# Kernel tuning notes

Measured on AMD Instinct MI355X. Metric: run time of the kernel, lower is better.

Reference implementation:

```python
import jax, jax.numpy as jnp
import numpy as np


def setup_inputs() -> dict:
    key = jax.random.key(0)
    ks = jax.random.split(key, 8)
    B, S, P = 512, 128, 32            # batch, seq_len, pred_len
    F, O, H = 64, 64, 1024            # feat_dim, label/output_dim, hidden_dim
    IN = F + O                        # GRUCell input_dim = 128
    w = 0.05                          # weight scale to keep gates in useful range
    return {
        "feats": jax.random.normal(ks[0], (B, S + P - 1, F), jnp.float32),
        "labels": jax.random.normal(ks[1], (B, S, O), jnp.float32),
        "Wi": jax.random.normal(ks[2], (3 * H, IN), jnp.float32) * w,
        "Wh": jax.random.normal(ks[3], (3 * H, H), jnp.float32) * w,
        "bi": jax.random.normal(ks[4], (3 * H,), jnp.float32) * w,
        "bh": jax.random.normal(ks[5], (3 * H,), jnp.float32) * w,
        "Wd": jax.random.normal(ks[6], (O, H), jnp.float32) * w,
        "bd": jax.random.normal(ks[7], (O,), jnp.float32) * w,
    }


def _gru_cell(h, x, Wi, Wh, bi, bh):
    # torch.nn.GRUCell semantics
    gi = x @ Wi.T + bi                       # [B, 3H]
    gh = h @ Wh.T + bh                       # [B, 3H]
    i_r, i_z, i_n = jnp.split(gi, 3, axis=-1)
    h_r, h_z, h_n = jnp.split(gh, 3, axis=-1)
    r = jax.nn.sigmoid(i_r + h_r)
    z = jax.nn.sigmoid(i_z + h_z)
    n = jnp.tanh(i_n + r * h_n)
    return (1.0 - z) * n + z * h


def reference(feats, labels, Wi, Wh, bi, bh, Wd, bd):
    B, S, O = labels.shape
    H = Wh.shape[1]
    prior = feats[:, :S]                     # [B, S, F]
    post = feats[:, S:]                      # [B, P-1, F]
    x = jnp.concatenate([prior, labels], axis=-1)   # [B, S, F+O]

    h0 = jnp.zeros((B, H), feats.dtype)

    def enc_step(h, xt):
        return _gru_cell(h, xt, Wi, Wh, bi, bh), None

    h, _ = jax.lax.scan(enc_step, h0, jnp.swapaxes(x, 0, 1))

    ps = h @ Wd.T + bd                       # decoder output [B, O]

    def dec_step(carry, ft):
        h, ps = carry
        xin = jnp.concatenate([ft, ps], axis=-1)
        h = _gru_cell(h, xin, Wi, Wh, bi, bh)
        ps = h @ Wd.T + bd
        return (h, ps), ps

    _, rest = jax.lax.scan(dec_step, (h, ps), jnp.swapaxes(post, 0, 1))
    return jnp.concatenate([ps[None], rest], axis=0)  # [pred_len, B, O]
```

## Files before the change

kernel.cpp:

```cpp
#include <hip/hip_runtime.h>
#include <cstdint>
#include <cstddef>

#define SENC  128
#define NSTEPS 159
#define HB16  524288
#define XSLICE 131072
#define SLAB_ELEMS 55296
#define FRAG_TOTAL 442368
#define FS 16

typedef short  short8  __attribute__((ext_vector_type(8)));
typedef float  floatx4 __attribute__((ext_vector_type(4)));
typedef float  f32x4   __attribute__((ext_vector_type(4)));
typedef int    i32x4   __attribute__((ext_vector_type(4)));
typedef unsigned long long u64;

#define MFMA(a, b, c) __builtin_amdgcn_mfma_f32_16x16x32_bf16((a), (b), (c), 0, 0, 0)

__device__ __forceinline__ i32x4 ld_nc16(const void* p) {
    i32x4 r;
    asm volatile("global_load_dwordx4 %0, %1, off sc0 sc1" : "=&v"(r) : "v"(p) : "memory");
    return r;
}
__device__ __forceinline__ i32x4 ld_sc0_16(const void* p) {
    i32x4 r;
    asm volatile("global_load_dwordx4 %0, %1, off sc0" : "=&v"(r) : "v"(p) : "memory");
    return r;
}
__device__ __forceinline__ void st_swap8(void* p, u64 v) {
    asm volatile("global_atomic_swap_x2 %0, %1, off sc1" :: "v"(p), "v"(v) : "memory");
}
__device__ __forceinline__ void st_swap4(void* p, unsigned v) {
    asm volatile("global_atomic_swap %0, %1, off sc1" :: "v"(p), "v"(v) : "memory");
}
#define WAITVM(N) asm volatile("s_waitcnt vmcnt(" #N ")" ::: "memory")
#define WAITLGKM  asm volatile("s_waitcnt lgkmcnt(0)" ::: "memory")

__device__ __forceinline__ unsigned ldu_dev(const unsigned* p) {
    return __hip_atomic_load(p, __ATOMIC_RELAXED, __HIP_MEMORY_SCOPE_AGENT);
}
__device__ __forceinline__ u64 ldq_dev(const u64* p) {
    return __hip_atomic_load(p, __ATOMIC_RELAXED, __HIP_MEMORY_SCOPE_AGENT);
}
__device__ __forceinline__ void stu_dev(unsigned* p, unsigned v) {
    __hip_atomic_store(p, v, __ATOMIC_RELAXED, __HIP_MEMORY_SCOPE_AGENT);
}

__device__ __forceinline__ unsigned ld_ws(const unsigned* p) {
    return __hip_atomic_load(p, __ATOMIC_RELAXED, __HIP_MEMORY_SCOPE_WORKGROUP);
}
__device__ __forceinline__ void st_ws(unsigned* p, unsigned v) {
    __hip_atomic_store(p, v, __ATOMIC_RELAXED, __HIP_MEMORY_SCOPE_WORKGROUP);
}
__device__ __forceinline__ unsigned add_ws(unsigned* p, unsigned v) {
    return __hip_atomic_fetch_add(p, v, __ATOMIC_RELAXED, __HIP_MEMORY_SCOPE_WORKGROUP);
}

__device__ __forceinline__ float bf2f(short s) {
    return __uint_as_float(((unsigned)(unsigned short)s) << 16);
}
__device__ __forceinline__ short f2bf(float f) {
    unsigned u = __float_as_uint(f);
    return (short)((u + 0x7FFFu + ((u >> 16) & 1u)) >> 16);
}
__device__ __forceinline__ void f2pair(float f, short& hi, short& lo) {
    hi = f2bf(f);
    lo = f2bf(f - bf2f(hi));
}

__device__ __forceinline__ float sigm(float x) {
    return 1.0f / (1.0f + __expf(-x));
}
__device__ __forceinline__ float tanh_fast(float x) {
    float cx = fminf(fmaxf(x, -15.0f), 15.0f);
    float e = __expf(2.0f * cx);
    return (e - 1.0f) / (e + 1.0f);
}

__global__ void setup_swizzle(const float* __restrict__ Wi, const float* __restrict__ Wh,
                              short* __restrict__ whi, short* __restrict__ wlo_x) {
    const int idx = blockIdx.x * 256 + threadIdx.x;
    if (idx >= FRAG_TOTAL) return;
    const int l    = idx & 63;
    const int rest = idx >> 6;
    const int t    = rest % 3;
    const int ki   = (rest / 3) % 36;
    const int c    = rest / 108;
    const int nrow = t * 1024 + c * 16 + (l & 15);
    const int kb   = ki * 32 + (l >> 4) * 8;
    short8 vh, vl;
#pragma unroll
    for (int j = 0; j < 8; ++j) {
        const int k = kb + j;
        float w = (k < 128) ? Wi[(size_t)nrow * 128 + k]
                            : Wh[(size_t)nrow * 1024 + (k - 128)];
        short h, lo2;
        f2pair(w, h, lo2);
        vh[j] = h; vl[j] = lo2;
    }
    *(short8*)(whi + (size_t)idx * 8) = vh;
    if (ki < 4) {
        const int xi = ((c * 4 + ki) * 3 + t) * 64 + l;
        *(short8*)(wlo_x + (size_t)xi * 8) = vl;
    }
}

#define HCONS(S, KI) do { \
    short8 ah_ = *(short8*)&hb[S]; \
    const int fo_ = (((KI) * 3) * 64 + lane) * 8; \
    short8 b0_ = *(const short8*)(s_whi + fo_); \
    short8 b1_ = *(const short8*)(s_whi + fo_ + 512); \
    short8 b2_ = *(const short8*)(s_whi + fo_ + 1024); \
    aR  = MFMA(ah_, b0_, aR); \
    aZ  = MFMA(ah_, b1_, aZ); \
    aNh = MFMA(ah_, b2_, aNh); \
} while (0)

#define CH_ISSUE(LDFN, B, KC) do { \
    const short* hp_ = hrd + (size_t)(KC) * 16384; \
    hb[(B) + 0] = LDFN(hp_); \
    hb[(B) + 1] = LDFN(hp_ + 4096); \
    hb[(B) + 2] = LDFN(hp_ + 8192); \
    hb[(B) + 3] = LDFN(hp_ + 12288); \
} while (0)

#define CH_CONS(B, KC) do { \
    const int kb_ = 4 + 4 * (KC); \
    HCONS((B) + 0, kb_ + 0); \
    HCONS((B) + 1, kb_ + 1); \
    HCONS((B) + 2, kb_ + 2); \
    HCONS((B) + 3, kb_ + 3); \
} while (0)

#define SPIN_CH(KC) do { \
    while (ld_ws(&s_sub[KC]) < (unsigned)step) __builtin_amdgcn_s_sleep(2); \
} while (0)

#define REGION2(LDFN) do { \
    i32x4 hb[16]; \
    const int k0_ = r0;            const int k1_ = (r0 + 1) & 7; \
    const int k2_ = (r0 + 2) & 7;  const int k3_ = (r0 + 3) & 7; \
    const int k4_ = (r0 + 4) & 7;  const int k5_ = (r0 + 5) & 7; \
    const int k6_ = (r0 + 6) & 7;  const int k7_ = (r0 + 7) & 7; \
    SPIN_CH(k0_); CH_ISSUE(LDFN, 0,  k0_); \
    SPIN_CH(k1_); CH_ISSUE(LDFN, 4,  k1_); \
    SPIN_CH(k2_); CH_ISSUE(LDFN, 8,  k2_); \
    SPIN_CH(k3_); CH_ISSUE(LDFN, 12, k3_); \
    WAITVM(12); CH_CONS(0,  k0_); SPIN_CH(k4_); CH_ISSUE(LDFN, 0,  k4_); \
    WAITVM(12); CH_CONS(4,  k1_); SPIN_CH(k5_); CH_ISSUE(LDFN, 4,  k5_); \
    WAITVM(12); CH_CONS(8,  k2_); SPIN_CH(k6_); CH_ISSUE(LDFN, 8,  k6_); \
    WAITVM(12); CH_CONS(12, k3_); SPIN_CH(k7_); CH_ISSUE(LDFN, 12, k7_); \
    WAITVM(12); CH_CONS(0,  k4_); \
    WAITVM(8);  CH_CONS(4,  k5_); \
    WAITVM(4);  CH_CONS(8,  k6_); \
    WAITVM(0);  CH_CONS(12, k7_); \
} while (0)

#define R1TRIPLE(KI) do { \
    short8 ah_, al_; \
    _Pragma("unroll") \
    for (int j = 0; j < 8; ++j) { short h2_, l2_; f2pair(f[j], h2_, l2_); ah_[j] = h2_; al_[j] = l2_; } \
    const int fo_ = (((KI) * 3) * 64 + lane) * 8; \
    short8 b0_ = *(const short8*)(s_whi + fo_); \
    short8 b1_ = *(const short8*)(s_whi + fo_ + 512); \
    short8 b2_ = *(const short8*)(s_whi + fo_ + 1024); \
    aR  = MFMA(ah_, b0_, aR);  aR  = MFMA(ah_, L0r[KI], aR);  aR  = MFMA(al_, b0_, aR); \
    aZ  = MFMA(ah_, b1_, aZ);  aZ  = MFMA(ah_, L1r[KI], aZ);  aZ  = MFMA(al_, b1_, aZ); \
    aNi = MFMA(ah_, b2_, aNi); aNi = MFMA(ah_, L2r[KI], aNi); aNi = MFMA(al_, b2_, aNi); \
} while (0)

#define LOADF(KI) do { \
    const float* s_ = feats + ((size_t)brow * 159 + step) * 64 + (KI) * 32 + q * 8; \
    f32x4 a_ = ((const f32x4*)s_)[0], b_ = ((const f32x4*)s_)[1]; \
    _Pragma("unroll") for (int j = 0; j < 4; ++j) { f[j] = a_[j]; f[4 + j] = b_[j]; } \
} while (0)

#define LOADL(KI) do { \
    const float* s_ = labels + ((size_t)brow * 128 + step) * 64 + ((KI) - 2) * 32 + q * 8; \
    f32x4 a_ = ((const f32x4*)s_)[0], b_ = ((const f32x4*)s_)[1]; \
    _Pragma("unroll") for (int j = 0; j < 4; ++j) { f[j] = a_[j]; f[4 + j] = b_[j]; } \
} while (0)

#define LOADP(KI) do { \
    const u64* pp_ = (const u64*)(ps_f32 + (size_t)brow * 64 + ((KI) - 2) * 32 + q * 8); \
    _Pragma("unroll") for (int j = 0; j < 4; ++j) { \
        u64 v_ = ldq_dev(pp_ + j); \
        f[2 * j]     = __uint_as_float((unsigned)v_); \
        f[2 * j + 1] = __uint_as_float((unsigned)(v_ >> 32)); } \
} while (0)

__global__ __launch_bounds__(512, 2) void gru_main(
    const float* __restrict__ feats, const float* __restrict__ labels,
    const float* __restrict__ bi,    const float* __restrict__ bh,
    const float* __restrict__ Wd,    const float* __restrict__ bd,
    const short* __restrict__ whi_sw, const short* __restrict__ wlo_x,
    short* __restrict__ h16,         float* __restrict__ ps_f32,
    float* __restrict__ out,
    unsigned* __restrict__ hflag,
    unsigned* __restrict__ pflag,
    int nslots)
{
    __shared__ short s_whi[SLAB_ELEMS];
    __shared__ float s_ps[2048];
    __shared__ short s_tr[8][16][18];
    __shared__ unsigned s_sub[8];
    __shared__ unsigned s_arrD, s_arrI;

    const int tid  = threadIdx.x;
    const int lane = tid & 63;
    const int wv   = tid >> 6;
    const int q    = lane >> 4;
    const int n16  = lane & 15;
    const int c    = blockIdx.x & 63;
    const int r    = blockIdx.x >> 6;
    const int r0   = c & 7;
    const bool cached = (nslots > 2);

    if (tid < 8) s_sub[tid] = 0;
    if (tid == 8) s_arrD = 0;
    if (tid == 9) s_arrI = 0;
    {
        const f32x4* src = (const f32x4*)(whi_sw + (size_t)c * SLAB_ELEMS);
        f32x4* dst = (f32x4*)s_whi;
        for (int i = tid; i < SLAB_ELEMS / 8; i += 512) dst[i] = src[i];
    }
    __syncthreads();

    const int mbase = r * 128 + wv * 16;
    const int brow  = mbase + n16;
    const int row_r = c * 16 + n16;
    const float bias_r  = bi[row_r] + bh[row_r];
    const float bias_z  = bi[1024 + row_r] + bh[1024 + row_r];
    const float bias_ni = bi[2048 + row_r];
    const float bias_nh = bh[2048 + row_r];

    unsigned* my_hflag = hflag + (r * 64 + c) * FS;
    unsigned* my_pflag = pflag + (r * 64 + c) * FS;
    const unsigned* hfp     = hflag + (r * 64 + 8 * wv + (lane & 7)) * FS;
    const unsigned* pfp     = pflag + (r * 64 + 8 * wv + (lane & 7)) * FS;
    const unsigned* grp_hfl = hflag + (r * 64) * FS;

    short8 L0r[4], L1r[4], L2r[4];
#pragma unroll
    for (int ki = 0; ki < 4; ++ki) {
        const short* base = wlo_x + (size_t)(((c * 4 + ki) * 3) * 64 + lane) * 8;
        L0r[ki] = *(const short8*)(base);
        L1r[ki] = *(const short8*)(base + 512);
        L2r[ki] = *(const short8*)(base + 1024);
    }

    float hold[4] = {0.f, 0.f, 0.f, 0.f};

    for (int step = 0; step < NSTEPS; ++step) {
        const bool dec = (step >= SENC);
        const unsigned tgt = (unsigned)(step + 1);
        const int rslot = cached ? step       : (step & 1);
        const int wslot = cached ? (step + 1) : ((step + 1) & 1);
        const short* hrd = h16 + (size_t)rslot * HB16 + (size_t)r * XSLICE
                         + (size_t)(wv * 16 + n16) * 16 + (q & 1) * 8 + (q >> 1) * 2048;
        short* hwr = h16 + (size_t)wslot * HB16 + (size_t)r * XSLICE;

        unsigned pf_pre = 0xFFFFFFFFu;
        if (dec) pf_pre = ldu_dev(pfp);

        floatx4 aR  = (floatx4){bias_r,  bias_r,  bias_r,  bias_r};
        floatx4 aZ  = (floatx4){bias_z,  bias_z,  bias_z,  bias_z};
        floatx4 aNi = (floatx4){bias_ni, bias_ni, bias_ni, bias_ni};
        floatx4 aNh = (floatx4){bias_nh, bias_nh, bias_nh, bias_nh};

        {
            float f[8];
            LOADF(0); R1TRIPLE(0);
            LOADF(1); R1TRIPLE(1);

            if (step > 0 && step <= SENC - 1) {
                WAITVM(0);
                if (lane == 0) {
                    unsigned old = add_ws(&s_arrD, 1u);
                    if (old == 8u * (unsigned)step - 1u)
                        stu_dev(my_hflag, (unsigned)step);
                }
            }

            if (!dec) {
                LOADL(2); R1TRIPLE(2);
                LOADL(3); R1TRIPLE(3);
            } else {
                if (!__all(pf_pre >= (unsigned)step)) {
                    while (!__all(ldu_dev(pfp) >= (unsigned)step))
                        __builtin_amdgcn_s_sleep(2);
                }
                LOADP(2); R1TRIPLE(2);
                LOADP(3); R1TRIPLE(3);
            }
        }

        if (step > 0) {
            if (!dec) {
                while (!__all(ldu_dev(hfp) >= (unsigned)step))
                    __builtin_amdgcn_s_sleep(2);
            }
            if (lane == 0) st_ws(&s_sub[wv], (unsigned)step);
            if (cached) { REGION2(ld_sc0_16); }
            else        { REGION2(ld_nc16); }
        }

        {
#pragma unroll
            for (int i = 0; i < 4; ++i) {
                float rr = sigm(aR[i]);
                float zz = sigm(aZ[i]);
                float nn = tanh_fast(aNi[i] + rr * aNh[i]);
                float hv = (1.0f - zz) * nn + zz * hold[i];
                hold[i] = hv;
                s_tr[wv][q * 4 + i][n16] = f2bf(hv);
            }
            WAITLGKM;
            const int rr2 = lane >> 2, seg = lane & 3;
            u64 v = *(const u64*)&s_tr[wv][rr2][seg * 4];
            st_swap8(hwr + (size_t)c * 2048 + (size_t)(wv * 16 + rr2) * 16 + seg * 4, v);
            if (step >= SENC - 1) {
                WAITVM(0);
                if (lane == 0) {
                    unsigned old = add_ws(&s_arrI, 1u);
                    if (old == 8u * (unsigned)(step - (SENC - 1) + 1) - 1u)
                        stu_dev(my_hflag, tgt);
                }
            }
        }

        if (step >= SENC - 1) {
            const int ot = step - (SENC - 1);
            const int prow0 = r * 128 + 2 * c;
            if (wv == 0) {
                while (ldu_dev(grp_hfl + lane * FS) < tgt)
                    __builtin_amdgcn_s_sleep(2);
            }
            __syncthreads();
            if (tid < 256) {
                const int rl = tid >> 7, rest = tid & 127;
                const int ct = rest >> 1, half = rest & 1;
                const short* src = hwr + (size_t)ct * 2048
                                 + (size_t)(2 * c + rl) * 16 + half * 8;
                i32x4 v = ld_nc16(src);
                WAITVM(0);
                short8 s = *(short8*)&v;
#pragma unroll
                for (int j = 0; j < 8; ++j)
                    s_ps[rl * 1024 + ct * 16 + half * 8 + j] = bf2f(s[j]);
            }
            __syncthreads();
            const int o = tid >> 3, e = tid & 7;
            const float* wrow = Wd + (size_t)o * 1024;
            float acc0 = 0.0f, acc1 = 0.0f;
#pragma unroll 8
            for (int j = 0; j < 32; ++j) {
                const int k = j * 32 + e * 4;
                f32x4 w  = *(const f32x4*)(wrow + k);
                f32x4 a4 = *(const f32x4*)(s_ps + k);
                f32x4 b4 = *(const f32x4*)(s_ps + 1024 + k);
                acc0 += a4[0] * w[0] + a4[1] * w[1] + a4[2] * w[2] + a4[3] * w[3];
                acc1 += b4[0] * w[0] + b4[1] * w[1] + b4[2] * w[2] + b4[3] * w[3];
            }
            acc0 += __shfl_xor(acc0, 1); acc0 += __shfl_xor(acc0, 2); acc0 += __shfl_xor(acc0, 4);
            acc1 += __shfl_xor(acc1, 1); acc1 += __shfl_xor(acc1, 2); acc1 += __shfl_xor(acc1, 4);
            if (e == 0) {
                float v0 = acc0 + bd[o];
                float v1 = acc1 + bd[o];
                out[((size_t)ot * 512 + prow0)     * 64 + o] = v0;
                out[((size_t)ot * 512 + prow0 + 1) * 64 + o] = v1;
                st_swap4(ps_f32 + (size_t)prow0       * 64 + o, __float_as_uint(v0));
                st_swap4(ps_f32 + (size_t)(prow0 + 1) * 64 + o, __float_as_uint(v1));
            }
            WAITVM(0);
            __syncthreads();
            if (tid == 0) stu_dev(my_pflag, tgt);
        }
    }
}

extern "C" void kernel_launch(void* const* d_in, const int* in_sizes, int n_in,
                              void* d_out, int out_size, void* d_ws, size_t ws_size,
                              hipStream_t stream) {
    const float* feats  = (const float*)d_in[0];
    const float* labels = (const float*)d_in[1];
    const float* Wi     = (const float*)d_in[2];
    const float* Wh     = (const float*)d_in[3];
    const float* bi     = (const float*)d_in[4];
    const float* bh     = (const float*)d_in[5];
    const float* Wd     = (const float*)d_in[6];
    const float* bd     = (const float*)d_in[7];
    float* out = (float*)d_out;

    char* ws = (char*)d_ws;
    short*    whi_sw = (short*)(ws);
    short*    wlo_x  = (short*)(ws + 7077888);
    float*    ps_f32 = (float*)(ws + 7864320);
    unsigned* pflag  = (unsigned*)(ws + 7995392);
    unsigned* hflag  = (unsigned*)(ws + 8011776);
    short*    h16    = (short*)(ws + 8388608);

    const size_t need = 8388608ull + 160ull * 1048576ull;
    int nslots = (ws_size >= need) ? 160 : 2;

    hipMemsetAsync(ws + 7995392, 0, 32768, stream);

    setup_swizzle<<<FRAG_TOTAL / 256, 256, 0, stream>>>(Wi, Wh, whi_sw, wlo_x);

    void* args[] = {(void*)&feats, (void*)&labels, (void*)&bi, (void*)&bh,
                    (void*)&Wd, (void*)&bd, (void*)&whi_sw, (void*)&wlo_x,
                    (void*)&h16, (void*)&ps_f32, (void*)&out,
                    (void*)&hflag, (void*)&pflag, (void*)&nslots};
    hipLaunchCooperativeKernel(reinterpret_cast<void*>(gru_main),
                               dim3(256), dim3(512), args, 0, stream);
}
```

Before: 1.410 ms.

## Split each block into two independent wave chains with per-chain flags

```diff
diff --git a/kernel.cpp b/kernel.cpp
--- a/kernel.cpp
+++ b/kernel.cpp
@@ -134,7 +134,7 @@
 } while (0)
 
 #define SPIN_CH(KC) do { \
-    while (ld_ws(&s_sub[KC]) < (unsigned)step) __builtin_amdgcn_s_sleep(2); \
+    while (ld_ws(&s_sub2[CHN][(KC) >> 1]) < (unsigned)step) __builtin_amdgcn_s_sleep(2); \
 } while (0)
 
 #define REGION2(LDFN) do { \
@@ -190,6 +190,12 @@
         f[2 * j + 1] = __uint_as_float((unsigned)(v_ >> 32)); } \
 } while (0)
 
+#define CHAIN_SYNC() do { \
+    cs_tgt += 4u; \
+    if (lane == 0) add_ws(&s_cs[CHN], 1u); \
+    while (ld_ws(&s_cs[CHN]) < cs_tgt) __builtin_amdgcn_s_sleep(1); \
+} while (0)
+
 __global__ __launch_bounds__(512, 2) void gru_main(
     const float* __restrict__ feats, const float* __restrict__ labels,
     const float* __restrict__ bi,    const float* __restrict__ bh,
@@ -204,28 +210,39 @@
     __shared__ short s_whi[SLAB_ELEMS];
     __shared__ float s_ps[2048];
     __shared__ short s_tr[8][16][18];
-    __shared__ unsigned s_sub[8];
-    __shared__ unsigned s_arrD, s_arrI;
+    __shared__ unsigned s_sub2[2][4];
+    __shared__ unsigned s_arrD2[2];
+    __shared__ unsigned s_arrI2[2];
+    __shared__ unsigned s_cs[2];
 
     const int tid  = threadIdx.x;
     const int lane = tid & 63;
     const int wv   = tid >> 6;
+    const int CHN  = wv >> 2;
+    const int wv4  = wv & 3;
     const int q    = lane >> 4;
     const int n16  = lane & 15;
     const int c    = blockIdx.x & 63;
     const int r    = blockIdx.x >> 6;
     const int r0   = c & 7;
     const bool cached = (nslots > 2);
-
-    if (tid < 8) s_sub[tid] = 0;
-    if (tid == 8) s_arrD = 0;
-    if (tid == 9) s_arrI = 0;
+    unsigned cs_tgt = 0;
+
+    if (tid < 8)   s_sub2[tid >> 2][tid & 3] = 0;
+    if (tid == 8)  s_arrD2[0] = 0;
+    if (tid == 9)  s_arrD2[1] = 0;
+    if (tid == 10) s_arrI2[0] = 0;
+    if (tid == 11) s_arrI2[1] = 0;
+    if (tid == 12) s_cs[0] = 0;
+    if (tid == 13) s_cs[1] = 0;
     {
         const f32x4* src = (const f32x4*)(whi_sw + (size_t)c * SLAB_ELEMS);
         f32x4* dst = (f32x4*)s_whi;
         for (int i = tid; i < SLAB_ELEMS / 8; i += 512) dst[i] = src[i];
     }
     __syncthreads();
+
+    if (CHN == 1) { __builtin_amdgcn_s_sleep(127); __builtin_amdgcn_s_sleep(32); }
 
     const int mbase = r * 128 + wv * 16;
     const int brow  = mbase + n16;
@@ -235,11 +252,10 @@
     const float bias_ni = bi[2048 + row_r];
     const float bias_nh = bh[2048 + row_r];
 
-    unsigned* my_hflag = hflag + (r * 64 + c) * FS;
+    unsigned* my_hflag = hflag + (((r * 64 + c) * 2) + CHN) * FS;
     unsigned* my_pflag = pflag + (r * 64 + c) * FS;
-    const unsigned* hfp     = hflag + (r * 64 + 8 * wv + (lane & 7)) * FS;
-    const unsigned* pfp     = pflag + (r * 64 + 8 * wv + (lane & 7)) * FS;
-    const unsigned* grp_hfl = hflag + (r * 64) * FS;
+    const unsigned* hfp16 = hflag + (((r * 64 + 16 * wv4 + (lane & 15)) * 2) + CHN) * FS;
+    const unsigned* pfp   = pflag + (r * 64 + 8 * wv + (lane & 7)) * FS;
 
     short8 L0r[4], L1r[4], L2r[4];
 #pragma unroll
@@ -277,8 +293,8 @@
             if (step > 0 && step <= SENC - 1) {
                 WAITVM(0);
                 if (lane == 0) {
-                    unsigned old = add_ws(&s_arrD, 1u);
-                    if (old == 8u * (unsigned)step - 1u)
+                    unsigned old = add_ws(&s_arrD2[CHN], 1u);
+                    if (old == 4u * (unsigned)step - 1u)
                         stu_dev(my_hflag, (unsigned)step);
                 }
             }
@@ -297,11 +313,9 @@
         }
 
         if (step > 0) {
-            if (!dec) {
-                while (!__all(ldu_dev(hfp) >= (unsigned)step))
-                    __builtin_amdgcn_s_sleep(2);
-            }
-            if (lane == 0) st_ws(&s_sub[wv], (unsigned)step);
+            while (!__all(ldu_dev(hfp16) >= (unsigned)step))
+                __builtin_amdgcn_s_sleep(2);
+            if (lane == 0) st_ws(&s_sub2[CHN][wv4], (unsigned)step);
             if (cached) { REGION2(ld_sc0_16); }
             else        { REGION2(ld_nc16); }
         }
@@ -323,23 +337,22 @@
             if (step >= SENC - 1) {
                 WAITVM(0);
                 if (lane == 0) {
-                    unsigned old = add_ws(&s_arrI, 1u);
-                    if (old == 8u * (unsigned)(step - (SENC - 1) + 1) - 1u)
+                    unsigned old = add_ws(&s_arrI2[CHN], 1u);
+                    if (old == 4u * (unsigned)(step - (SENC - 1) + 1) - 1u)
                         stu_dev(my_hflag, tgt);
                 }
             }
         }
 
-        if (step >= SENC - 1) {
+        if (step >= SENC - 1 && CHN == (c >> 5)) {
             const int ot = step - (SENC - 1);
             const int prow0 = r * 128 + 2 * c;
-            if (wv == 0) {
-                while (ldu_dev(grp_hfl + lane * FS) < tgt)
-                    __builtin_amdgcn_s_sleep(2);
-            }
-            __syncthreads();
-            if (tid < 256) {
-                const int rl = tid >> 7, rest = tid & 127;
+            while (!__all(ldu_dev(hfp16) >= tgt))
+                __builtin_amdgcn_s_sleep(2);
+            CHAIN_SYNC();
+            {
+                const int ctid = wv4 * 64 + lane;
+                const int rl = ctid >> 7, rest = ctid & 127;
                 const int ct = rest >> 1, half = rest & 1;
                 const short* src = hwr + (size_t)ct * 2048
                                  + (size_t)(2 * c + rl) * 16 + half * 8;
@@ -350,21 +363,22 @@
                 for (int j = 0; j < 8; ++j)
                     s_ps[rl * 1024 + ct * 16 + half * 8 + j] = bf2f(s[j]);
             }
-            __syncthreads();
-            const int o = tid >> 3, e = tid & 7;
+            CHAIN_SYNC();
+            const int ctid = wv4 * 64 + lane;
+            const int o = ctid >> 2, e = ctid & 3;
             const float* wrow = Wd + (size_t)o * 1024;
             float acc0 = 0.0f, acc1 = 0.0f;
 #pragma unroll 8
-            for (int j = 0; j < 32; ++j) {
-                const int k = j * 32 + e * 4;
+            for (int j = 0; j < 64; ++j) {
+                const int k = j * 16 + e * 4;
                 f32x4 w  = *(const f32x4*)(wrow + k);
                 f32x4 a4 = *(const f32x4*)(s_ps + k);
                 f32x4 b4 = *(const f32x4*)(s_ps + 1024 + k);
                 acc0 += a4[0] * w[0] + a4[1] * w[1] + a4[2] * w[2] + a4[3] * w[3];
                 acc1 += b4[0] * w[0] + b4[1] * w[1] + b4[2] * w[2] + b4[3] * w[3];
             }
-            acc0 += __shfl_xor(acc0, 1); acc0 += __shfl_xor(acc0, 2); acc0 += __shfl_xor(acc0, 4);
-            acc1 += __shfl_xor(acc1, 1); acc1 += __shfl_xor(acc1, 2); acc1 += __shfl_xor(acc1, 4);
+            acc0 += __shfl_xor(acc0, 1); acc0 += __shfl_xor(acc0, 2);
+            acc1 += __shfl_xor(acc1, 1); acc1 += __shfl_xor(acc1, 2);
             if (e == 0) {
                 float v0 = acc0 + bd[o];
                 float v1 = acc1 + bd[o];
@@ -374,8 +388,8 @@
                 st_swap4(ps_f32 + (size_t)(prow0 + 1) * 64 + o, __float_as_uint(v1));
             }
             WAITVM(0);
-            __syncthreads();
-            if (tid == 0) stu_dev(my_pflag, tgt);
+            CHAIN_SYNC();
+            if (wv4 == 0 && lane == 0) stu_dev(my_pflag, tgt);
         }
     }
 }
@@ -404,7 +418,7 @@
     const size_t need = 8388608ull + 160ull * 1048576ull;
     int nslots = (ws_size >= need) ? 160 : 2;
 
-    hipMemsetAsync(ws + 7995392, 0, 32768, stream);
+    hipMemsetAsync(ws + 7995392, 0, 49152, stream);
 
     setup_swizzle<<<FRAG_TOTAL / 256, 256, 0, stream>>>(Wi, Wh, whi_sw, wlo_x);
 
```

New measurement: 1.612 ms. 14.4% more time.
